# Optimization experiments

Hardware: AMD Instinct MI355X
Metric: run time of the kernel (lower is better)

The kernel has to match this reference:

```python
import jax, jax.numpy as jnp
import numpy as np

GAMMAS = jnp.array([2.7, 2.1, 2.4, 2.0, 3.0, 2.9, 3.0, 2.5, 2.1, 2.6, 2.0, 2.1, 2.7, 2.4, 2.2], dtype=jnp.float32)

B, NCLS, H, W = 32, 15, 256, 256
K, CREG = 500, 2


def setup_inputs() -> dict:
    key = jax.random.key(0)
    ks = jax.random.split(key, 6)
    pred = jax.random.uniform(ks[0], (B, NCLS, H, W), dtype=jnp.float32)
    gt = jax.random.uniform(ks[1], (B, NCLS, H, W), dtype=jnp.float32)
    output = jax.random.normal(ks[2], (B, CREG, H, W), dtype=jnp.float32)
    mask = jax.random.randint(ks[3], (B, K), 0, 2, dtype=jnp.int32)
    ind = jax.random.randint(ks[4], (B, K), 0, H * W)
    target = jax.random.normal(ks[5], (B, K, CREG), dtype=jnp.float32)
    inde = jax.random.randint(jax.random.fold_in(key, 7), (B, K, 3), 0, 15)
    return {"pred": pred, "gt": gt, "output": output, "mask": mask,
            "ind": ind, "target": target, "inde": inde}


def _forward(pred, gt, output, mask, ind, target, inde):
    b, c_out = output.shape[0], output.shape[1]
    k = ind.shape[1]
    # _tranpose_and_gather_feat: [B,C,H,W] -> [B,HW,C], gather along dim 1
    feat = jnp.transpose(output, (0, 2, 3, 1)).reshape(b, -1, c_out)
    pre = jnp.take_along_axis(feat, ind[:, :, None].astype(jnp.int32), axis=1)  # [B,K,C]

    d = pre - target
    ad = jnp.abs(d)
    huber = jnp.where(ad < 1.0, 0.5 * d * d, ad - 0.5)
    l_bk = huber.mean(axis=2)  # [B,K]

    pos_mask = mask.astype(bool)
    factor = jnp.arctan(l_bk) * (2.0 / jnp.pi)
    vals = jnp.where(pos_mask, factor, 1.0).reshape(-1)

    b_idx = jnp.broadcast_to(jnp.arange(b)[:, None], (b, k)).reshape(-1)
    ch = inde[..., 0].reshape(-1)
    yy = inde[..., 1].reshape(-1)
    xx = inde[..., 2].reshape(-1)
    # in-place multiplicative scatter; torch's pred_uni aliases pred so the
    # modified tensor is used for BOTH pred_cat and pred_cat_uni below
    pred_mod = pred.at[b_idx, ch, yy, xx].multiply(vals)

    # loss is overwritten each loop iteration in the original: only the LAST
    # positive's smooth-L1 loss survives (0 if no positives)
    flat_m = pos_mask.reshape(-1)
    flat_l = l_bk.reshape(-1)
    last = jnp.max(jnp.where(flat_m, jnp.arange(flat_m.shape[0]), -1))
    loss0 = jnp.where(last >= 0, flat_l[jnp.clip(last, 0)], 0.0)

    # focal term, vectorized over the 15 class channels
    eps = 1e-12
    g = GAMMAS[None, :, None, None]
    pos_inds = (gt == 1.0).astype(pred.dtype)
    neg_inds = (gt < 1.0).astype(pred.dtype)
    neg_weights = jnp.power(1.0 - gt, 4)
    pos_loss = jnp.log(pred_mod + eps) * jnp.power(1.0 - pred_mod, g) * pos_inds
    neg_loss = jnp.log(1.0 - pred_mod + eps) * jnp.power(pred_mod, g) * neg_weights * neg_inds
    per_ch = jnp.sum(pos_loss + neg_loss, axis=(0, 2, 3))  # [15]
    loss = loss0 - jnp.sum(per_ch * GAMMAS * 0.5)

    num_pos = pos_inds.sum()
    return jnp.where(num_pos == 0, loss, loss / num_pos)


def reference(pred, gt, output, mask, ind, target, inde):
    return _forward(pred, gt, output, mask, ind, target, inde)
```

## Files before the change

### kernel.cpp

```cpp
#include <hip/hip_runtime.h>
#include <math.h>

#define BB 32
#define NCLS 15
#define HH 256
#define WW 256
#define KK 500
#define HW (HH*WW)
#define NELEM (BB*NCLS*HW)
#define N4 (NELEM/4)
#define NSLOT (NCLS*16*16)

#define AUXB 32
#define FG (AUXB + 1920)
#define FT 256
#define SLAB4 16384
#define QUART 4096

typedef float v4f __attribute__((ext_vector_type(4)));

__constant__ float c_gammas[15] = {2.7f,2.1f,2.4f,2.0f,3.0f,2.9f,3.0f,2.5f,
                                   2.1f,2.6f,2.0f,2.1f,2.7f,2.4f,2.2f};

#define EXP2F(x) __builtin_amdgcn_exp2f(x)
#define LOG2F(x) __builtin_amdgcn_logf(x)
#define LN2 0.69314718055994530942f

__device__ float g_S = 0.0f;
__device__ float g_np = 0.0f;
__device__ unsigned long long g_lastpack = 0ULL;
__device__ unsigned int g_count = 0u;

__device__ __forceinline__ float elem(float p, float g, float gam, float& np) {
    float t    = 1.0f - g;
    float t2   = t * t;
    float negw = (g < 1.0f) ? t2 * t2 : 0.0f;
    float pw   = EXP2F(gam * LOG2F(p));
    float v    = (LN2 * LOG2F(1.0f - p + 1e-12f)) * pw * negw;
    if (g == 1.0f) {
        np += 1.0f;
        v += (LN2 * LOG2F(p + 1e-12f)) * EXP2F(gam * LOG2F(1.0f - p));
    }
    return v;
}

__device__ __forceinline__ float elem4(v4f p, v4f g, float gam, float& np) {
    return elem(p.x, g.x, gam, np) + elem(p.y, g.y, gam, np)
         + elem(p.z, g.z, gam, np) + elem(p.w, g.w, gam, np);
}

__device__ __forceinline__ float blockReduceSum(float v) {
    __shared__ float sh[4];
    #pragma unroll
    for (int o = 32; o > 0; o >>= 1) v += __shfl_down(v, o);
    int lane = threadIdx.x & 63, w = threadIdx.x >> 6;
    if (lane == 0) sh[w] = v;
    __syncthreads();
    float r = 0.0f;
    if (threadIdx.x == 0) r = sh[0] + sh[1] + sh[2] + sh[3];
    __syncthreads();
    return r;
}

__global__ __launch_bounds__(256) void k_mega(const v4f*   __restrict__ pred4,
                                              const v4f*   __restrict__ gt4,
                                              const float* __restrict__ pred,
                                              const float* __restrict__ gt,
                                              const float* __restrict__ output,
                                              const int*   __restrict__ mask,
                                              const int*   __restrict__ ind,
                                              const float* __restrict__ target,
                                              const int*   __restrict__ inde,
                                              float* out) {
    __shared__ float shM[NSLOT];
    __shared__ unsigned long long shL[4];
    const int tid = threadIdx.x;
    const int blk = blockIdx.x;

    float acc = 0.0f;
    float np  = 0.0f;

    if (blk < AUXB) {
        const int b = blk;
        for (int i = tid; i < NSLOT; i += FT) shM[i] = 1.0f;
        __syncthreads();

        unsigned long long lp = 0ULL;
        for (int k = tid; k < KK; k += FT) {
            int t = b * KK + k;
            int pos = ind[t];
            const float* ob = output + (size_t)b * 2 * HW;
            float p0 = ob[pos];
            float p1 = ob[HW + pos];
            float d0 = p0 - target[t*2 + 0];
            float d1 = p1 - target[t*2 + 1];
            float a0 = fabsf(d0), a1 = fabsf(d1);
            float h0 = (a0 < 1.0f) ? 0.5f*d0*d0 : a0 - 0.5f;
            float h1 = (a1 < 1.0f) ? 0.5f*d1*d1 : a1 - 0.5f;
            float l  = 0.5f * (h0 + h1);
            if (mask[t] != 0) {
                unsigned long long pk =
                    ((unsigned long long)(unsigned)(t + 1) << 32) |
                    (unsigned long long)__float_as_uint(l);
                lp = (pk > lp) ? pk : lp;
                float factor = atanf(l) * 0.63661977236758134308f;
                int ch = inde[t*3 + 0];
                int yy = inde[t*3 + 1];
                int xx = inde[t*3 + 2];
                int mi = (ch*16 + yy)*16 + xx;
                unsigned int* addr = (unsigned int*)&shM[mi];
                unsigned int old = *addr, assumed;
                do {
                    assumed = old;
                    float nv = __uint_as_float(assumed) * factor;
                    old = atomicCAS(addr, assumed, __float_as_uint(nv));
                } while (old != assumed);
            }
        }
        #pragma unroll
        for (int o = 32; o > 0; o >>= 1) {
            unsigned long long other = __shfl_down(lp, o);
            lp = (other > lp) ? other : lp;
        }
        int lane = tid & 63, w = tid >> 6;
        if (lane == 0) shL[w] = lp;
        __syncthreads();
        if (tid == 0) {
            unsigned long long m0 = shL[0] > shL[1] ? shL[0] : shL[1];
            unsigned long long m1 = shL[2] > shL[3] ? shL[2] : shL[3];
            unsigned long long mm = m0 > m1 ? m0 : m1;
            if (mm) atomicMax(&g_lastpack, mm);
        }
        __syncthreads();

        for (int i = tid; i < NSLOT; i += FT) {
            float m = shM[i];
            if (m != 1.0f) {
                int ch = i >> 8;
                int yy = (i >> 4) & 15;
                int xx = i & 15;
                size_t off = ((size_t)(b*NCLS + ch) << 16) + (yy*WW + xx);
                float p = pred[off];
                float g = gt[off];
                float gam = c_gammas[ch];
                float dmy = 0.0f;
                acc += gam * (elem(p*m, g, gam, dmy) - elem(p, g, gam, dmy));
            }
        }
    } else {
        const int sblk = blk - AUXB;
        const int slab = sblk >> 2;
        const int c    = slab % NCLS;
        const float gam = c_gammas[c];
        const int base = slab * SLAB4 + (sblk & 3) * QUART + tid;

        float sacc = 0.0f;
        #pragma unroll 1
        for (int k = 0; k < 4; ++k) {
            int i0 = base + k * 1024;
            v4f p0 = __builtin_nontemporal_load(pred4 + i0);
            v4f g0 = __builtin_nontemporal_load(gt4   + i0);
            v4f p1 = __builtin_nontemporal_load(pred4 + i0 + 256);
            v4f g1 = __builtin_nontemporal_load(gt4   + i0 + 256);
            v4f p2 = __builtin_nontemporal_load(pred4 + i0 + 512);
            v4f g2 = __builtin_nontemporal_load(gt4   + i0 + 512);
            v4f p3 = __builtin_nontemporal_load(pred4 + i0 + 768);
            v4f g3 = __builtin_nontemporal_load(gt4   + i0 + 768);
            sacc += elem4(p0, g0, gam, np);
            sacc += elem4(p1, g1, gam, np);
            sacc += elem4(p2, g2, gam, np);
            sacc += elem4(p3, g3, gam, np);
        }
        acc = gam * sacc;
    }

    float bs = blockReduceSum(acc);
    float bn = blockReduceSum(np);
    if (tid == 0) {
        if (bs != 0.0f) atomicAdd(&g_S, bs);
        if (bn != 0.0f) atomicAdd(&g_np, bn);
        __threadfence();
        unsigned int done = atomicAdd(&g_count, 1u);
        if (done % FG == FG - 1) {
            float S   = atomicAdd(&g_S, 0.0f);
            float npv = atomicAdd(&g_np, 0.0f);
            unsigned long long lpv = atomicAdd(&g_lastpack, 0ULL);
            float loss0 = (lpv >> 32) ?
                __uint_as_float((unsigned int)(lpv & 0xffffffffu)) : 0.0f;
            float loss = loss0 - 0.5f * S;
            out[0] = (npv == 0.0f) ? loss : loss / npv;
            atomicExch(&g_S, 0.0f);
            atomicExch(&g_np, 0.0f);
            atomicExch(&g_lastpack, 0ULL);
        }
    }
}

extern "C" void kernel_launch(void* const* d_in, const int* in_sizes, int n_in,
                              void* d_out, int out_size, void* d_ws, size_t ws_size,
                              hipStream_t stream) {
    const float* pred   = (const float*)d_in[0];
    const float* gt     = (const float*)d_in[1];
    const float* output = (const float*)d_in[2];
    const int*   mask   = (const int*)d_in[3];
    const int*   ind    = (const int*)d_in[4];
    const float* target = (const float*)d_in[5];
    const int*   inde   = (const int*)d_in[6];
    float* out = (float*)d_out;
    (void)d_ws; (void)ws_size;

    k_mega<<<FG, FT, 0, stream>>>((const v4f*)pred, (const v4f*)gt,
                                  pred, gt, output, mask, ind, target, inde,
                                  out);
}
```

Measured before the change: 349.2 us.

## Split aux scatter into separate kernel and double-buffer streaming loads

The small scatter/smooth-L1 work moves into its own 32-block kernel launched before the streaming kernel. The streaming kernel now uses 960 blocks, each covering half a slab with 8 chunks instead of 4. It software-pipelines the loads with two register sets and sched barriers so the next chunk's loads are in flight while the current chunk is computed. This aims to hide memory latency and keep the bulk kernel uniform, at the cost of a second launch, higher register pressure and fewer blocks.

New measurement: 296.1 us. 1.18x faster.

```diff
diff --git a/kernel.cpp b/kernel.cpp
--- a/kernel.cpp
+++ b/kernel.cpp
@@ -11,11 +11,10 @@
 #define N4 (NELEM/4)
 #define NSLOT (NCLS*16*16)
 
-#define AUXB 32
-#define FG (AUXB + 1920)
+#define FG 960
 #define FT 256
 #define SLAB4 16384
-#define QUART 4096
+#define HALF4 8192
 
 typedef float v4f __attribute__((ext_vector_type(4)));
 
@@ -62,117 +61,126 @@
     return r;
 }
 
-__global__ __launch_bounds__(256) void k_mega(const v4f*   __restrict__ pred4,
-                                              const v4f*   __restrict__ gt4,
-                                              const float* __restrict__ pred,
-                                              const float* __restrict__ gt,
-                                              const float* __restrict__ output,
-                                              const int*   __restrict__ mask,
-                                              const int*   __restrict__ ind,
-                                              const float* __restrict__ target,
-                                              const int*   __restrict__ inde,
-                                              float* out) {
+__global__ __launch_bounds__(256) void k_aux(const float* __restrict__ pred,
+                                             const float* __restrict__ gt,
+                                             const float* __restrict__ output,
+                                             const int*   __restrict__ mask,
+                                             const int*   __restrict__ ind,
+                                             const float* __restrict__ target,
+                                             const int*   __restrict__ inde) {
     __shared__ float shM[NSLOT];
     __shared__ unsigned long long shL[4];
     const int tid = threadIdx.x;
+    const int b   = blockIdx.x;
+
+    for (int i = tid; i < NSLOT; i += FT) shM[i] = 1.0f;
+    __syncthreads();
+
+    unsigned long long lp = 0ULL;
+    for (int k = tid; k < KK; k += FT) {
+        int t = b * KK + k;
+        int pos = ind[t];
+        const float* ob = output + (size_t)b * 2 * HW;
+        float p0 = ob[pos];
+        float p1 = ob[HW + pos];
+        float d0 = p0 - target[t*2 + 0];
+        float d1 = p1 - target[t*2 + 1];
+        float a0 = fabsf(d0), a1 = fabsf(d1);
+        float h0 = (a0 < 1.0f) ? 0.5f*d0*d0 : a0 - 0.5f;
+        float h1 = (a1 < 1.0f) ? 0.5f*d1*d1 : a1 - 0.5f;
+        float l  = 0.5f * (h0 + h1);
+        if (mask[t] != 0) {
+            unsigned long long pk =
+                ((unsigned long long)(unsigned)(t + 1) << 32) |
+                (unsigned long long)__float_as_uint(l);
+            lp = (pk > lp) ? pk : lp;
+            float factor = atanf(l) * 0.63661977236758134308f;
+            int ch = inde[t*3 + 0];
+            int yy = inde[t*3 + 1];
+            int xx = inde[t*3 + 2];
+            int mi = (ch*16 + yy)*16 + xx;
+            unsigned int* addr = (unsigned int*)&shM[mi];
+            unsigned int old = *addr, assumed;
+            do {
+                assumed = old;
+                float nv = __uint_as_float(assumed) * factor;
+                old = atomicCAS(addr, assumed, __float_as_uint(nv));
+            } while (old != assumed);
+        }
+    }
+    #pragma unroll
+    for (int o = 32; o > 0; o >>= 1) {
+        unsigned long long other = __shfl_down(lp, o);
+        lp = (other > lp) ? other : lp;
+    }
+    int lane = tid & 63, w = tid >> 6;
+    if (lane == 0) shL[w] = lp;
+    __syncthreads();
+    if (tid == 0) {
+        unsigned long long m0 = shL[0] > shL[1] ? shL[0] : shL[1];
+        unsigned long long m1 = shL[2] > shL[3] ? shL[2] : shL[3];
+        unsigned long long mm = m0 > m1 ? m0 : m1;
+        if (mm) atomicMax(&g_lastpack, mm);
+    }
+
+    float acc = 0.0f, dmy = 0.0f;
+    for (int i = tid; i < NSLOT; i += FT) {
+        float m = shM[i];
+        if (m != 1.0f) {
+            int ch = i >> 8;
+            int yy = (i >> 4) & 15;
+            int xx = i & 15;
+            size_t off = ((size_t)(b*NCLS + ch) << 16) + (size_t)(yy*WW + xx);
+            float p = pred[off];
+            float g = gt[off];
+            float gam = c_gammas[ch];
+            acc += gam * (elem(p*m, g, gam, dmy) - elem(p, g, gam, dmy));
+        }
+    }
+    float bs = blockReduceSum(acc);
+    if (tid == 0 && bs != 0.0f) atomicAdd(&g_S, bs);
+}
+
+#define NTL(p) __builtin_nontemporal_load(p)
+#define SB __builtin_amdgcn_sched_barrier(0);
+
+#define PREF(P,G,off) \
+    P##0 = NTL(pb + (off));       G##0 = NTL(gb + (off)); \
+    P##1 = NTL(pb + (off) + 256); G##1 = NTL(gb + (off) + 256); \
+    P##2 = NTL(pb + (off) + 512); G##2 = NTL(gb + (off) + 512); \
+    P##3 = NTL(pb + (off) + 768); G##3 = NTL(gb + (off) + 768);
+
+#define COMP(P,G) \
+    sacc += elem4(P##0, G##0, gam, np); sacc += elem4(P##1, G##1, gam, np); \
+    sacc += elem4(P##2, G##2, gam, np); sacc += elem4(P##3, G##3, gam, np);
+
+__global__ __launch_bounds__(256) void k_stream(const v4f* __restrict__ pred4,
+                                                const v4f* __restrict__ gt4,
+                                                float* out) {
+    const int tid = threadIdx.x;
     const int blk = blockIdx.x;
 
-    float acc = 0.0f;
-    float np  = 0.0f;
-
-    if (blk < AUXB) {
-        const int b = blk;
-        for (int i = tid; i < NSLOT; i += FT) shM[i] = 1.0f;
-        __syncthreads();
-
-        unsigned long long lp = 0ULL;
-        for (int k = tid; k < KK; k += FT) {
-            int t = b * KK + k;
-            int pos = ind[t];
-            const float* ob = output + (size_t)b * 2 * HW;
-            float p0 = ob[pos];
-            float p1 = ob[HW + pos];
-            float d0 = p0 - target[t*2 + 0];
-            float d1 = p1 - target[t*2 + 1];
-            float a0 = fabsf(d0), a1 = fabsf(d1);
-            float h0 = (a0 < 1.0f) ? 0.5f*d0*d0 : a0 - 0.5f;
-            float h1 = (a1 < 1.0f) ? 0.5f*d1*d1 : a1 - 0.5f;
-            float l  = 0.5f * (h0 + h1);
-            if (mask[t] != 0) {
-                unsigned long long pk =
-                    ((unsigned long long)(unsigned)(t + 1) << 32) |
-                    (unsigned long long)__float_as_uint(l);
-                lp = (pk > lp) ? pk : lp;
-                float factor = atanf(l) * 0.63661977236758134308f;
-                int ch = inde[t*3 + 0];
-                int yy = inde[t*3 + 1];
-                int xx = inde[t*3 + 2];
-                int mi = (ch*16 + yy)*16 + xx;
-                unsigned int* addr = (unsigned int*)&shM[mi];
-                unsigned int old = *addr, assumed;
-                do {
-                    assumed = old;
-                    float nv = __uint_as_float(assumed) * factor;
-                    old = atomicCAS(addr, assumed, __float_as_uint(nv));
-                } while (old != assumed);
-            }
-        }
-        #pragma unroll
-        for (int o = 32; o > 0; o >>= 1) {
-            unsigned long long other = __shfl_down(lp, o);
-            lp = (other > lp) ? other : lp;
-        }
-        int lane = tid & 63, w = tid >> 6;
-        if (lane == 0) shL[w] = lp;
-        __syncthreads();
-        if (tid == 0) {
-            unsigned long long m0 = shL[0] > shL[1] ? shL[0] : shL[1];
-            unsigned long long m1 = shL[2] > shL[3] ? shL[2] : shL[3];
-            unsigned long long mm = m0 > m1 ? m0 : m1;
-            if (mm) atomicMax(&g_lastpack, mm);
-        }
-        __syncthreads();
-
-        for (int i = tid; i < NSLOT; i += FT) {
-            float m = shM[i];
-            if (m != 1.0f) {
-                int ch = i >> 8;
-                int yy = (i >> 4) & 15;
-                int xx = i & 15;
-                size_t off = ((size_t)(b*NCLS + ch) << 16) + (yy*WW + xx);
-                float p = pred[off];
-                float g = gt[off];
-                float gam = c_gammas[ch];
-                float dmy = 0.0f;
-                acc += gam * (elem(p*m, g, gam, dmy) - elem(p, g, gam, dmy));
-            }
-        }
-    } else {
-        const int sblk = blk - AUXB;
-        const int slab = sblk >> 2;
-        const int c    = slab % NCLS;
-        const float gam = c_gammas[c];
-        const int base = slab * SLAB4 + (sblk & 3) * QUART + tid;
-
-        float sacc = 0.0f;
-        #pragma unroll 1
-        for (int k = 0; k < 4; ++k) {
-            int i0 = base + k * 1024;
-            v4f p0 = __builtin_nontemporal_load(pred4 + i0);
-            v4f g0 = __builtin_nontemporal_load(gt4   + i0);
-            v4f p1 = __builtin_nontemporal_load(pred4 + i0 + 256);
-            v4f g1 = __builtin_nontemporal_load(gt4   + i0 + 256);
-            v4f p2 = __builtin_nontemporal_load(pred4 + i0 + 512);
-            v4f g2 = __builtin_nontemporal_load(gt4   + i0 + 512);
-            v4f p3 = __builtin_nontemporal_load(pred4 + i0 + 768);
-            v4f g3 = __builtin_nontemporal_load(gt4   + i0 + 768);
-            sacc += elem4(p0, g0, gam, np);
-            sacc += elem4(p1, g1, gam, np);
-            sacc += elem4(p2, g2, gam, np);
-            sacc += elem4(p3, g3, gam, np);
-        }
-        acc = gam * sacc;
-    }
+    const int slab = blk >> 1;
+    const int c    = slab % NCLS;
+    const float gam = c_gammas[c];
+    const v4f* pb = pred4 + slab * SLAB4 + (blk & 1) * HALF4 + tid;
+    const v4f* gb = gt4   + slab * SLAB4 + (blk & 1) * HALF4 + tid;
+
+    float sacc = 0.0f, np = 0.0f;
+    v4f pA0, pA1, pA2, pA3, gA0, gA1, gA2, gA3;
+    v4f pB0, pB1, pB2, pB3, gB0, gB1, gB2, gB3;
+
+    PREF(pA, gA, 0)
+    PREF(pB, gB, 1024) SB COMP(pA, gA)
+    PREF(pA, gA, 2048) SB COMP(pB, gB)
+    PREF(pB, gB, 3072) SB COMP(pA, gA)
+    PREF(pA, gA, 4096) SB COMP(pB, gB)
+    PREF(pB, gB, 5120) SB COMP(pA, gA)
+    PREF(pA, gA, 6144) SB COMP(pB, gB)
+    PREF(pB, gB, 7168) SB COMP(pA, gA)
+    COMP(pB, gB)
+
+    float acc = gam * sacc;
 
     float bs = blockReduceSum(acc);
     float bn = blockReduceSum(np);
@@ -209,7 +217,6 @@
     float* out = (float*)d_out;
     (void)d_ws; (void)ws_size;
 
-    k_mega<<<FG, FT, 0, stream>>>((const v4f*)pred, (const v4f*)gt,
-                                  pred, gt, output, mask, ind, target, inde,
-                                  out);
-}
+    k_aux   <<<BB, FT, 0, stream>>>(pred, gt, output, mask, ind, target, inde);
+    k_stream<<<FG, FT, 0, stream>>>((const v4f*)pred, (const v4f*)gt, out);
+}
```
